# Optimization experiments

Measured on AMD Instinct MI355X. Metric: run time of the kernel, lower is better.

Reference implementation:

```python
import jax, jax.numpy as jnp
import numpy as np

B, N1, N2 = 2, 2048, 8192
IN_F, OUT_F = 128, 64
ALPHA = 0.2
NEG = -9e15


def setup_inputs() -> dict:
    key = jax.random.key(0)
    ks = jax.random.split(key, 8)
    stdv = 1.0 / np.sqrt(OUT_F)
    x = jax.random.normal(ks[0], (B, N2, IN_F), dtype=jnp.float32)
    adj = (jax.random.uniform(ks[1], (B, N1, N2)) < 0.05).astype(jnp.float32)
    u = lambda k, shp: jax.random.uniform(k, shp, minval=-stdv, maxval=stdv, dtype=jnp.float32)
    W2 = u(ks[2], (IN_F, OUT_F))
    W3 = u(ks[3], (OUT_F, OUT_F))
    a = u(ks[4], (2 * OUT_F, 1))
    a2 = u(ks[5], (2 * OUT_F, 1))
    word_ctx = u(ks[6], (OUT_F,))
    return {"x": x, "adj": adj, "W2": W2, "W3": W3, "a": a, "a2": a2, "word_ctx": word_ctx}


def reference(x, adj, W2, W3, a, a2, word_ctx):
    F_out = W2.shape[1]
    x4 = jnp.einsum('bnf,fo->bno', x, W2)            # [B, N2, F] node features for attention
    mask = adj > 0                                     # [B, N1, N2]
    # --- stage 1: edge-level attention over member nodes (softmax over N2) ---
    # pair score = leakyrelu([word_ctx, x4_j] @ a); independent of hyperedge index i
    a_q, a_x = a[:F_out, 0], a[F_out:, 0]
    s1 = jax.nn.leaky_relu(jnp.dot(word_ctx, a_q) + x4 @ a_x, ALPHA)  # [B, N2]
    e1 = jnp.where(mask, s1[:, None, :], NEG)          # [B, N1, N2]
    att_edge = jax.nn.softmax(e1, axis=2)
    edge = jnp.einsum('bij,bjf->bif', att_edge, x4)    # [B, N1, F]
    edge4 = jnp.einsum('bif,fo->bio', edge, W3)        # [B, N1, F]
    # --- stage 2: node-level attention over incident hyperedges (softmax over N1) ---
    a2_x, a2_e = a2[:F_out, 0], a2[F_out:, 0]
    s2 = jax.nn.leaky_relu((edge4 @ a2_e)[:, :, None] + (x4 @ a2_x)[:, None, :], ALPHA)  # [B, N1, N2]
    e2 = jnp.where(mask, s2, NEG)
    att_node = jax.nn.softmax(jnp.transpose(e2, (0, 2, 1)), axis=2)  # [B, N2, N1]
    node = jnp.einsum('bji,bif->bjf', att_node, edge4)               # [B, N2, F]
    return node, edge
```

## Files before the change

kernel.cpp:

```cpp
#include <hip/hip_runtime.h>
#include <stdint.h>

#define NB 2
#define N1 2048
#define N2 8192
#define INF_ 128
#define F 64
#define ALPHA 0.2f
#define CAP_E 640
#define CAP_N 192

__global__ __launch_bounds__(256) void k_mask_csr(
    const float4* __restrict__ adj4, uint64_t* __restrict__ bits,
    uint16_t* __restrict__ idxE, int* __restrict__ cntE)
{
    __shared__ uint16_t sIdx[4][CAP_E];
    __shared__ uint64_t sBits[4][128];
    int tid  = threadIdx.x;
    int lane = tid & 63;
    int wv   = tid >> 6;
    int row  = blockIdx.x * 4 + wv;
    int b    = row >> 11;
    const float4* ar = adj4 + (size_t)row * (N2 / 4) + lane;
    uint64_t* bw = bits + (size_t)row * (N2 / 64);
    uint16_t* sp = sIdx[wv];
    uint64_t lmask = (1ull << lane) - 1;
    int base = 0;

#define EMIT(vv, g2i) {                                                        \
    int jb = (g2i) * 256 + 4 * lane;                                           \
    unsigned long long m0 = __ballot(vv.x != 0.0f);                            \
    unsigned long long m1 = __ballot(vv.y != 0.0f);                            \
    unsigned long long m2 = __ballot(vv.z != 0.0f);                            \
    unsigned long long m3 = __ballot(vv.w != 0.0f);                            \
    if (vv.x != 0.0f) sp[base + (int)__popcll(m0 & lmask)] = (uint16_t)jb;     \
    base += (int)__popcll(m0);                                                 \
    if (vv.y != 0.0f) sp[base + (int)__popcll(m1 & lmask)] = (uint16_t)(jb+1); \
    base += (int)__popcll(m1);                                                 \
    if (vv.z != 0.0f) sp[base + (int)__popcll(m2 & lmask)] = (uint16_t)(jb+2); \
    base += (int)__popcll(m2);                                                 \
    if (vv.w != 0.0f) sp[base + (int)__popcll(m3 & lmask)] = (uint16_t)(jb+3); \
    base += (int)__popcll(m3);                                                 \
    if (lane == 0) {                                                           \
        uint64_t* o = &sBits[wv][(g2i) * 4];                                   \
        o[0] = m0; o[1] = m1; o[2] = m2; o[3] = m3;                            \
    }                                                                          \
}

    float4 v0 = ar[0], v1 = ar[64], v2 = ar[128], v3 = ar[192];
    #pragma unroll
    for (int g2 = 0; g2 < 32; g2 += 4) {
        float4 n0, n1, n2, n3;
        if (g2 + 4 < 32) {
            n0 = ar[(g2 + 4) * 64]; n1 = ar[(g2 + 5) * 64];
            n2 = ar[(g2 + 6) * 64]; n3 = ar[(g2 + 7) * 64];
        }
        EMIT(v0, g2); EMIT(v1, g2 + 1); EMIT(v2, g2 + 2); EMIT(v3, g2 + 3);
        v0 = n0; v1 = n1; v2 = n2; v3 = n3;
    }
#undef EMIT
    int n = base;
    int padded = (n + 15) & ~15;
    if (padded > CAP_E) padded = CAP_E;
    uint16_t sent = (uint16_t)((NB - b) * N2);
    if (n + lane < padded) sp[n + lane] = sent;

    bw[lane]      = sBits[wv][lane];
    bw[64 + lane] = sBits[wv][64 + lane];
    const uint32_t* s32 = (const uint32_t*)sp;
    uint32_t* o32 = (uint32_t*)(idxE + (size_t)row * CAP_E);
    for (int d = lane; 2 * d < padded; d += 64) o32[d] = s32[d];
    if (lane == 0) cntE[row] = n;
}

__global__ __launch_bounds__(512) void k_x4(
    const float* __restrict__ x, const float* __restrict__ W2,
    const float* __restrict__ a, const float* __restrict__ a2,
    const float* __restrict__ wctx,
    float* __restrict__ y, float* __restrict__ w1, float* __restrict__ q)
{
    __shared__ float  w2s[INF_ * F];
    __shared__ float4 xs4[64 * 32];
    int tid  = threadIdx.x;
    int lane = tid & 63;
    int w    = tid >> 6;

    for (int idx = tid; idx < INF_ * F; idx += 512) w2s[idx] = W2[idx];
    if (blockIdx.x == 0) {
        if (tid < F) y[(size_t)NB * N2 * F + tid] = 0.f;
        if (tid == 0) w1[NB * N2] = 0.f;
    }
    {
        const float4* xg4 = (const float4*)(x + (size_t)blockIdx.x * 64 * INF_);
        int r  = tid >> 3;
        int c0 = (tid & 7) * 4;
        #pragma unroll
        for (int i = 0; i < 4; ++i)
            xs4[r * 32 + c0 + i] = xg4[r * 32 + c0 + i];
    }
    float cpart = wctx[lane] * a[lane];
    #pragma unroll
    for (int s = 32; s; s >>= 1) cpart += __shfl_xor(cpart, s);
    float ax  = a[64 + lane];
    float a2x = a2[lane];
    __syncthreads();

    float acc[8] = {0.f, 0.f, 0.f, 0.f, 0.f, 0.f, 0.f, 0.f};
    for (int k4 = 0; k4 < 32; ++k4) {
        float wk0 = w2s[(4 * k4 + 0) * F + lane];
        float wk1 = w2s[(4 * k4 + 1) * F + lane];
        float wk2 = w2s[(4 * k4 + 2) * F + lane];
        float wk3 = w2s[(4 * k4 + 3) * F + lane];
        #pragma unroll
        for (int r = 0; r < 8; ++r) {
            float4 xv = xs4[(8 * w + r) * 32 + k4];
            acc[r] = fmaf(xv.x, wk0, acc[r]);
            acc[r] = fmaf(xv.y, wk1, acc[r]);
            acc[r] = fmaf(xv.z, wk2, acc[r]);
            acc[r] = fmaf(xv.w, wk3, acc[r]);
        }
    }
    int row0 = blockIdx.x * 64 + 8 * w;
    #pragma unroll
    for (int r = 0; r < 8; ++r) {
        float acc_ = acc[r];
        float r1 = acc_ * ax, r2 = acc_ * a2x;
        #pragma unroll
        for (int s = 32; s; s >>= 1) { r1 += __shfl_xor(r1, s); r2 += __shfl_xor(r2, s); }
        float s1 = cpart + r1;
        s1 = fmaxf(s1, ALPHA * s1);
        float wv1 = __expf(s1);
        y[(size_t)(row0 + r) * F + lane] = wv1 * acc_;
        if (lane == 0) { w1[row0 + r] = wv1; q[row0 + r] = r2; }
    }
}

union SU {
    float w3[F * F];
    struct {
        uint16_t idxn[64][194];
        int      pre[4][64];
        int      cnt[64];
    } t;
};

__global__ __launch_bounds__(256) void kB2(
    const uint64_t* __restrict__ bits,
    uint16_t* __restrict__ idxN, int* __restrict__ cntN,
    const uint16_t* __restrict__ idxE, const int* __restrict__ cntE,
    const float* __restrict__ y, const float* __restrict__ w1,
    const float* __restrict__ W3, const float* __restrict__ a2,
    float* __restrict__ out_edge, float* __restrict__ edge4, float* __restrict__ p)
{
    __shared__ SU su;
    int tid  = threadIdx.x;
    int lane = tid & 63;
    int w    = tid >> 6;

    if (blockIdx.x < 256) {
        int b  = blockIdx.x >> 7;
        int jw = blockIdx.x & 127;
        const uint64_t Mtab[6] = {0x00000000FFFFFFFFull, 0x0000FFFF0000FFFFull,
                                  0x00FF00FF00FF00FFull, 0x0F0F0F0F0F0F0F0Full,
                                  0x3333333333333333ull, 0x5555555555555555ull};
        uint64_t wd[8];
        #pragma unroll
        for (int t = 0; t < 8; ++t) {
            int ib = w * 8 + t;
            uint64_t xv = bits[((size_t)(b * N1 + ib * 64 + lane)) * (N2 / 64) + jw];
            #pragma unroll
            for (int st = 0; st < 6; ++st) {
                int s = 32 >> st;
                uint64_t M = Mtab[st];
                uint64_t yy = (uint64_t)__shfl_xor((unsigned long long)xv, s);
                xv = ((lane & s) == 0) ? ((xv & M) | ((yy & M) << s))
                                       : ((xv & ~M) | ((yy & ~M) >> s));
            }
            wd[t] = xv;
        }
        int myc = 0;
        #pragma unroll
        for (int t = 0; t < 8; ++t) myc += (int)__popcll(wd[t]);
        su.t.pre[w][lane] = myc;
        __syncthreads();
        int c0 = su.t.pre[0][lane], c1 = su.t.pre[1][lane];
        int c2 = su.t.pre[2][lane], c3 = su.t.pre[3][lane];
        int base = (w > 0 ? c0 : 0) + (w > 1 ? c1 : 0) + (w > 2 ? c2 : 0);
        int total = c0 + c1 + c2 + c3;
        int n = total < CAP_N ? total : CAP_N;
        if (w == 0) su.t.cnt[lane] = n;

        uint16_t* sr = su.t.idxn[lane];
        int off = base;
        #pragma unroll
        for (int t = 0; t < 8; ++t) {
            uint64_t m = wd[t];
            int ibase = (w * 8 + t) << 6;
            while (m) {
                int ii = __builtin_ctzll(m); m &= m - 1;
                if (off < CAP_N) sr[off] = (uint16_t)(ibase + ii);
                ++off;
            }
        }
        int jp = jw * 64 + lane;
        int j  = ((jp >> 8) << 8) + ((jp & 63) << 2) + ((jp >> 6) & 3);
        int rowOut = b * N2 + j;
        if (w == 3) {
            int padded = (n + 15) & ~15;
            if (padded > CAP_N) padded = CAP_N;
            uint16_t sent = (uint16_t)((NB - b) * N1);
            for (int o = n; o < padded; ++o) sr[o] = sent;
            cntN[rowOut] = n;
        }
        __syncthreads();
        int jbase = b * N2 + ((jw >> 2) << 8) + (jw & 3);
        for (int rr = 0; rr < 16; ++rr) {
            int r = w * 16 + rr;
            int n_r = su.t.cnt[r];
            int padded_r = (n_r + 15) & ~15;
            if (padded_r > CAP_N) padded_r = CAP_N;
            int rowOut_r = jbase + r * 4;
            uint32_t* dst = (uint32_t*)(idxN + (size_t)rowOut_r * CAP_N);
            const uint32_t* src = (const uint32_t*)su.t.idxn[r];
            for (int d = lane; 2 * d < padded_r; d += 64) dst[d] = src[d];
        }
    } else {
        for (int idx = tid; idx < F * F; idx += blockDim.x) su.w3[idx] = W3[idx];
        if (blockIdx.x == 256 && tid == 0) p[NB * N1] = -1e30f;
        __syncthreads();
        int g    = lane >> 4;
        int sub  = lane & 15;
        float a2e = a2[64 + lane];
        int row = ((blockIdx.x - 256) * 256 + tid) >> 6;
        if (row >= NB * N1) return;
        int b = row >> 11;
        const float4* yb4 = (const float4*)(y + (size_t)b * N2 * F);
        const float*  w1b = w1 + (size_t)b * N2;
        const uint16_t* ix = idxE + (size_t)row * CAP_E;
        int n = cntE[row];
        int padded = (n + 15) & ~15;
        if (padded > CAP_E) padded = CAP_E;
        float4 acc = make_float4(0.f, 0.f, 0.f, 0.f);
        float zl = 0.f, zl4 = 0.f;
        int t = 0;
        for (; t + 64 <= padded; t += 64) {
            int myj = ix[t + lane];
            zl += w1b[myj];
            #pragma unroll
            for (int s = 0; s < 16; ++s) {
                int jv = __shfl(myj, 4 * s + g);
                float4 v = yb4[(size_t)jv * 16 + sub];
                acc.x += v.x; acc.y += v.y; acc.z += v.z; acc.w += v.w;
            }
        }
        for (; t < padded; t += 16) {
            int myj = ix[t + (lane & 15)];
            zl4 += w1b[myj];
            #pragma unroll
            for (int s = 0; s < 4; ++s) {
                int jv = __shfl(myj, 4 * s + g);
                float4 v = yb4[(size_t)jv * 16 + sub];
                acc.x += v.x; acc.y += v.y; acc.z += v.z; acc.w += v.w;
            }
        }
        #pragma unroll
        for (int s2 = 16; s2 <= 32; s2 <<= 1) {
            acc.x += __shfl_xor(acc.x, s2);
            acc.y += __shfl_xor(acc.y, s2);
            acc.z += __shfl_xor(acc.z, s2);
            acc.w += __shfl_xor(acc.w, s2);
        }
        float zc = zl + 0.25f * zl4;
        #pragma unroll
        for (int s2 = 32; s2; s2 >>= 1) zc += __shfl_xor(zc, s2);
        float inv = 1.f / zc;
        float4 ev4 = make_float4(acc.x * inv, acc.y * inv, acc.z * inv, acc.w * inv);
        if (lane < 16) ((float4*)out_edge)[(size_t)row * 16 + sub] = ev4;
        float e0 = __shfl(ev4.x, lane >> 2);
        float e1 = __shfl(ev4.y, lane >> 2);
        float e2 = __shfl(ev4.z, lane >> 2);
        float e3 = __shfl(ev4.w, lane >> 2);
        int c = lane & 3;
        float ev = (c == 0) ? e0 : (c == 1) ? e1 : (c == 2) ? e2 : e3;
        float acc4 = 0.f;
        #pragma unroll 8
        for (int gg = 0; gg < 64; ++gg) acc4 += __shfl(ev, gg) * su.w3[gg * F + lane];
        edge4[(size_t)row * F + lane] = acc4;
        float r = acc4 * a2e;
        #pragma unroll
        for (int s2 = 32; s2; s2 >>= 1) r += __shfl_xor(r, s2);
        if (lane == 0) p[row] = r;
    }
}

__global__ __launch_bounds__(256) void kE(
    const uint16_t* __restrict__ idxN, const int* __restrict__ cntN,
    const float* __restrict__ edge4, const float* __restrict__ p,
    const float* __restrict__ q, float* __restrict__ out_node)
{
    int lane = threadIdx.x & 63;
    int g    = lane >> 4;
    int sub  = lane & 15;
    int gw = (blockIdx.x * blockDim.x + threadIdx.x) >> 6;
    int nw = (gridDim.x * blockDim.x) >> 6;
    for (int row = gw; row < NB * N2; row += nw) {
        int b = row >> 13;
        const float4* e4b4 = (const float4*)(edge4 + (size_t)b * N1 * F);
        const float*  pb   = p + b * N1;
        const uint16_t* ix = idxN + (size_t)row * CAP_N;
        float qj = q[row];
        int n = cntN[row];
        int padded = (n + 15) & ~15;
        if (padded > CAP_N) padded = CAP_N;
        float4 acc = make_float4(0.f, 0.f, 0.f, 0.f);
        float zl = 0.f, zl4 = 0.f;
        int t = 0;
        for (; t + 64 <= padded; t += 64) {
            int myi = ix[t + lane];
            float sc = pb[myi] + qj;
            sc = fmaxf(sc, ALPHA * sc);
            float wl = __expf(sc);
            zl += wl;
            #pragma unroll
            for (int s = 0; s < 16; ++s) {
                int iv   = __shfl(myi, 4 * s + g);
                float wv = __shfl(wl,  4 * s + g);
                float4 v = e4b4[(size_t)iv * 16 + sub];
                acc.x = fmaf(wv, v.x, acc.x);
                acc.y = fmaf(wv, v.y, acc.y);
                acc.z = fmaf(wv, v.z, acc.z);
                acc.w = fmaf(wv, v.w, acc.w);
            }
        }
        for (; t < padded; t += 16) {
            int myi = ix[t + (lane & 15)];
            float sc = pb[myi] + qj;
            sc = fmaxf(sc, ALPHA * sc);
            float wl = __expf(sc);
            zl4 += wl;
            #pragma unroll
            for (int s = 0; s < 4; ++s) {
                int iv   = __shfl(myi, 4 * s + g);
                float wv = __shfl(wl,  4 * s + g);
                float4 v = e4b4[(size_t)iv * 16 + sub];
                acc.x = fmaf(wv, v.x, acc.x);
                acc.y = fmaf(wv, v.y, acc.y);
                acc.z = fmaf(wv, v.z, acc.z);
                acc.w = fmaf(wv, v.w, acc.w);
            }
        }
        #pragma unroll
        for (int s2 = 16; s2 <= 32; s2 <<= 1) {
            acc.x += __shfl_xor(acc.x, s2);
            acc.y += __shfl_xor(acc.y, s2);
            acc.z += __shfl_xor(acc.z, s2);
            acc.w += __shfl_xor(acc.w, s2);
        }
        float zc = zl + 0.25f * zl4;
        #pragma unroll
        for (int s2 = 32; s2; s2 >>= 1) zc += __shfl_xor(zc, s2);
        float inv = 1.f / zc;
        if (lane < 16) {
            float4 o = make_float4(acc.x * inv, acc.y * inv, acc.z * inv, acc.w * inv);
            ((float4*)out_node)[(size_t)row * 16 + sub] = o;
        }
    }
}

extern "C" void kernel_launch(void* const* d_in, const int* in_sizes, int n_in,
                              void* d_out, int out_size, void* d_ws, size_t ws_size,
                              hipStream_t stream)
{
    const float* x    = (const float*)d_in[0];
    const float* adj  = (const float*)d_in[1];
    const float* W2   = (const float*)d_in[2];
    const float* W3   = (const float*)d_in[3];
    const float* a    = (const float*)d_in[4];
    const float* a2   = (const float*)d_in[5];
    const float* wctx = (const float*)d_in[6];

    float* out      = (float*)d_out;
    float* node_out = out;
    float* edge_out = out + (size_t)NB * N2 * F;

    float* ws    = (float*)d_ws;
    float* y     = ws;
    float* w1    = y  + (size_t)NB * N2 * F + F;
    float* q     = w1 + (size_t)NB * N2 + 4;
    float* edge4 = q  + (size_t)NB * N2;
    float* p     = edge4 + (size_t)NB * N1 * F;
    uint64_t* bits = (uint64_t*)(p + NB * N1 + 4);
    int* cntE = (int*)(bits + (size_t)NB * N1 * (N2 / 64));
    int* cntN = cntE + NB * N1;
    uint16_t* idxE = (uint16_t*)(cntN + NB * N2);
    uint16_t* idxN = idxE + (size_t)NB * N1 * CAP_E;

    hipLaunchKernelGGL(k_mask_csr, dim3(1024), dim3(256), 0, stream,
                       (const float4*)adj, bits, idxE, cntE);
    hipLaunchKernelGGL(k_x4, dim3(NB * N2 / 64), dim3(512), 0, stream,
                       x, W2, a, a2, wctx, y, w1, q);
    hipLaunchKernelGGL(kB2, dim3(1280), dim3(256), 0, stream,
                       bits, idxN, cntN, idxE, cntE, y, w1, W3, a2,
                       edge_out, edge4, p);
    hipLaunchKernelGGL(kE, dim3(4096), dim3(256), 0, stream,
                       idxN, cntN, edge4, p, q, node_out);
}
```

Before: 101.9 us.

## Split each adjacency row across a whole block in mask-to-CSR kernel

The mask/CSR kernel now assigns one adjacency row to a 256-thread block instead of one row per wavefront. Each wave loads its quarter of the row with all eight loads issued up front, ballots into shared bitmasks and counts nonzeros. A block-level prefix over the four wave counts then lets each wave scatter its column indices into a shared list. This increases memory-level parallelism and the number of blocks for the bandwidth-bound adjacency scan, at the cost of two block barriers and a second pass over the bitmasks.

```diff
diff --git a/kernel.cpp b/kernel.cpp
--- a/kernel.cpp
+++ b/kernel.cpp
@@ -14,63 +14,65 @@
     const float4* __restrict__ adj4, uint64_t* __restrict__ bits,
     uint16_t* __restrict__ idxE, int* __restrict__ cntE)
 {
-    __shared__ uint16_t sIdx[4][CAP_E];
-    __shared__ uint64_t sBits[4][128];
+    __shared__ uint64_t sBits[128];
+    __shared__ uint16_t sIdx[CAP_E];
+    __shared__ int      sCnt[4];
     int tid  = threadIdx.x;
     int lane = tid & 63;
-    int wv   = tid >> 6;
-    int row  = blockIdx.x * 4 + wv;
+    int w    = tid >> 6;
+    int row  = blockIdx.x;
     int b    = row >> 11;
-    const float4* ar = adj4 + (size_t)row * (N2 / 4) + lane;
-    uint64_t* bw = bits + (size_t)row * (N2 / 64);
-    uint16_t* sp = sIdx[wv];
+
+    const float4* ar = adj4 + (size_t)row * (N2 / 4) + (size_t)w * 512 + lane;
+    float4 v[8];
+    #pragma unroll
+    for (int it = 0; it < 8; ++it) v[it] = ar[it * 64];
+    int cnt = 0;
+    #pragma unroll
+    for (int it = 0; it < 8; ++it) {
+        unsigned long long m0 = __ballot(v[it].x != 0.0f);
+        unsigned long long m1 = __ballot(v[it].y != 0.0f);
+        unsigned long long m2 = __ballot(v[it].z != 0.0f);
+        unsigned long long m3 = __ballot(v[it].w != 0.0f);
+        if (lane == 0) {
+            uint64_t* o = &sBits[w * 32 + it * 4];
+            o[0] = m0; o[1] = m1; o[2] = m2; o[3] = m3;
+        }
+        cnt += (int)__popcll(m0) + (int)__popcll(m1)
+             + (int)__popcll(m2) + (int)__popcll(m3);
+    }
+    if (lane == 0) sCnt[w] = cnt;
+    __syncthreads();
+
+    int c0 = sCnt[0], c1 = sCnt[1], c2 = sCnt[2], c3 = sCnt[3];
+    int base = (w > 0 ? c0 : 0) + (w > 1 ? c1 : 0) + (w > 2 ? c2 : 0);
+    int total = c0 + c1 + c2 + c3;
     uint64_t lmask = (1ull << lane) - 1;
-    int base = 0;
-
-#define EMIT(vv, g2i) {                                                        \
-    int jb = (g2i) * 256 + 4 * lane;                                           \
-    unsigned long long m0 = __ballot(vv.x != 0.0f);                            \
-    unsigned long long m1 = __ballot(vv.y != 0.0f);                            \
-    unsigned long long m2 = __ballot(vv.z != 0.0f);                            \
-    unsigned long long m3 = __ballot(vv.w != 0.0f);                            \
-    if (vv.x != 0.0f) sp[base + (int)__popcll(m0 & lmask)] = (uint16_t)jb;     \
-    base += (int)__popcll(m0);                                                 \
-    if (vv.y != 0.0f) sp[base + (int)__popcll(m1 & lmask)] = (uint16_t)(jb+1); \
-    base += (int)__popcll(m1);                                                 \
-    if (vv.z != 0.0f) sp[base + (int)__popcll(m2 & lmask)] = (uint16_t)(jb+2); \
-    base += (int)__popcll(m2);                                                 \
-    if (vv.w != 0.0f) sp[base + (int)__popcll(m3 & lmask)] = (uint16_t)(jb+3); \
-    base += (int)__popcll(m3);                                                 \
-    if (lane == 0) {                                                           \
-        uint64_t* o = &sBits[wv][(g2i) * 4];                                   \
-        o[0] = m0; o[1] = m1; o[2] = m2; o[3] = m3;                            \
-    }                                                                          \
-}
-
-    float4 v0 = ar[0], v1 = ar[64], v2 = ar[128], v3 = ar[192];
     #pragma unroll
-    for (int g2 = 0; g2 < 32; g2 += 4) {
-        float4 n0, n1, n2, n3;
-        if (g2 + 4 < 32) {
-            n0 = ar[(g2 + 4) * 64]; n1 = ar[(g2 + 5) * 64];
-            n2 = ar[(g2 + 6) * 64]; n3 = ar[(g2 + 7) * 64];
-        }
-        EMIT(v0, g2); EMIT(v1, g2 + 1); EMIT(v2, g2 + 2); EMIT(v3, g2 + 3);
-        v0 = n0; v1 = n1; v2 = n2; v3 = n3;
-    }
-#undef EMIT
-    int n = base;
+    for (int k = 0; k < 32; ++k) {
+        int wi = w * 32 + k;
+        uint64_t m = sBits[wi];
+        if ((m >> lane) & 1) {
+            int pos = base + (int)__popcll(m & lmask);
+            sIdx[pos] = (uint16_t)(((wi >> 2) << 8) + (lane << 2) + (wi & 3));
+        }
+        base += (int)__popcll(m);
+    }
+    int n = total;
     int padded = (n + 15) & ~15;
     if (padded > CAP_E) padded = CAP_E;
-    uint16_t sent = (uint16_t)((NB - b) * N2);
-    if (n + lane < padded) sp[n + lane] = sent;
-
-    bw[lane]      = sBits[wv][lane];
-    bw[64 + lane] = sBits[wv][64 + lane];
-    const uint32_t* s32 = (const uint32_t*)sp;
+    if (w == 3) {
+        uint16_t sent = (uint16_t)((NB - b) * N2);
+        if (n + lane < padded) sIdx[n + lane] = sent;
+    }
+    __syncthreads();
+
+    uint64_t* bw = bits + (size_t)row * (N2 / 64);
+    if (tid < 128) bw[tid] = sBits[tid];
+    const uint32_t* s32 = (const uint32_t*)sIdx;
     uint32_t* o32 = (uint32_t*)(idxE + (size_t)row * CAP_E);
-    for (int d = lane; 2 * d < padded; d += 64) o32[d] = s32[d];
-    if (lane == 0) cntE[row] = n;
+    for (int d = tid; 2 * d < padded; d += 256) o32[d] = s32[d];
+    if (tid == 0) cntE[row] = n;
 }
 
 __global__ __launch_bounds__(512) void k_x4(
@@ -395,7 +397,7 @@
     uint16_t* idxE = (uint16_t*)(cntN + NB * N2);
     uint16_t* idxN = idxE + (size_t)NB * N1 * CAP_E;
 
-    hipLaunchKernelGGL(k_mask_csr, dim3(1024), dim3(256), 0, stream,
+    hipLaunchKernelGGL(k_mask_csr, dim3(NB * N1), dim3(256), 0, stream,
                        (const float4*)adj, bits, idxE, cntE);
     hipLaunchKernelGGL(k_x4, dim3(NB * N2 / 64), dim3(512), 0, stream,
                        x, W2, a, a2, wctx, y, w1, q);
```

After: 102.6 us. No clear change (+0.7%).
